# Kernel tuning notes

Hardware: AMD Instinct MI355X
Metric: run time of the kernel (lower is better)

Reference implementation:

```python
import jax, jax.numpy as jnp
import numpy as np

B, N_ATOMS = 8192, 64      # molecules, atoms per molecule
DIM, EXTRA, N_CLS = 70, 7, 11
N_FP = 10000               # fingerprint vocab


def setup_inputs() -> dict:
    key = jax.random.key(0)
    ks = jax.random.split(key, 9)
    atoms = jax.random.randint(ks[0], (B, N_ATOMS), 0, N_FP, dtype=jnp.int64 if jax.config.jax_enable_x64 else jnp.int32)
    adjacency = jax.random.uniform(ks[1], (B, N_ATOMS, N_ATOMS), dtype=jnp.float32)
    sel_desc = jax.random.normal(ks[2], (B, EXTRA), dtype=jnp.float32)
    embed_table = jax.random.normal(ks[3], (N_FP, DIM), dtype=jnp.float32)
    w1 = jax.random.normal(ks[4], (DIM, DIM), dtype=jnp.float32) * 0.05
    b1 = jax.random.normal(ks[5], (DIM,), dtype=jnp.float32) * 0.05
    w2 = jax.random.normal(ks[6], (DIM, DIM), dtype=jnp.float32) * 0.05
    b2 = jax.random.normal(ks[7], (DIM,), dtype=jnp.float32) * 0.05
    wp = jax.random.normal(ks[8], (DIM + EXTRA, N_CLS), dtype=jnp.float32) * 0.05
    bp = jnp.zeros((N_CLS,), dtype=jnp.float32)
    return {"atoms": atoms, "adjacency": adjacency, "sel_desc": sel_desc,
            "embed_table": embed_table, "w1": w1, "b1": b1,
            "w2": w2, "b2": b2, "wp": wp, "bp": bp}


def reference(atoms, adjacency, sel_desc, embed_table, w1, b1, w2, b2, wp, bp):
    # embed atoms: [B, n, dim]
    x = embed_table[atoms]
    # message-passing layers: relu(linear) then (block-diagonal == batched) adjacency matmul
    for w, b in ((w1, b1), (w2, b2)):
        h = jax.nn.relu(jnp.einsum('bnd,de->bne', x, w) + b)
        x = jnp.einsum('bnm,bmd->bnd', adjacency, h)
    # segment-sum pool over atoms per molecule (sum_axis)
    y = jnp.sum(x, axis=1)                       # [B, dim]
    y = jnp.concatenate([y, sel_desc], axis=1)   # [B, dim+extra]
    return jnp.einsum('bd,dc->bc', y, wp) + bp   # [B, 11]
```

## Files before the change

kernel.cpp:

```cpp
#include <hip/hip_runtime.h>

#define NFP   10000
#define DIM   70
#define DPAD  72
#define NATOMS 64

typedef short  short8  __attribute__((ext_vector_type(8)));
typedef float  floatx4 __attribute__((ext_vector_type(4)));

__device__ inline unsigned short f2bf(float f) {
  union { float f; unsigned u; } x; x.f = f;
  unsigned r = x.u + 0x7fffu + ((x.u >> 16) & 1u);
  return (unsigned short)(r >> 16);
}

__global__ __launch_bounds__(256) void precompute_G(
    const float* __restrict__ emb, const float* __restrict__ w1,
    const float* __restrict__ b1,  const float* __restrict__ w2,
    unsigned short* __restrict__ G) {
  __shared__ float w1s[DIM * DPAD];
  __shared__ float w2s[DIM * DPAD];
  __shared__ float b1s[DPAD];
  __shared__ float embs[32 * DPAD];
  __shared__ float e1s[32 * DPAD];
  const int t = threadIdx.x;

  for (int i = t; i < DIM * DPAD; i += 256) {
    int r = i / DPAD, c = i % DPAD;
    float v1 = 0.f, v2 = 0.f;
    if (c < DIM) { v1 = w1[r * DIM + c]; v2 = w2[r * DIM + c]; }
    w1s[i] = v1; w2s[i] = v2;
  }
  if (t < DPAD) b1s[t] = (t < DIM) ? b1[t] : 0.f;
  const int row0 = blockIdx.x * 32;
  for (int i = t; i < 32 * DPAD; i += 256) {
    int r = i / DPAD, c = i % DPAD;
    int vr = row0 + r;
    embs[i] = (vr < NFP && c < DIM) ? emb[vr * DIM + c] : 0.f;
  }
  __syncthreads();

  for (int task = t; task < 32 * 18; task += 256) {
    int r = task / 18, c4 = (task % 18) * 4;
    float4 acc = *(const float4*)&b1s[c4];
    for (int k = 0; k < DIM; k++) {
      float e = embs[r * DPAD + k];
      float4 w = *(const float4*)&w1s[k * DPAD + c4];
      acc.x = fmaf(e, w.x, acc.x); acc.y = fmaf(e, w.y, acc.y);
      acc.z = fmaf(e, w.z, acc.z); acc.w = fmaf(e, w.w, acc.w);
    }
    acc.x = fmaxf(acc.x, 0.f); acc.y = fmaxf(acc.y, 0.f);
    acc.z = fmaxf(acc.z, 0.f); acc.w = fmaxf(acc.w, 0.f);
    *(float4*)&e1s[r * DPAD + c4] = acc;
  }
  __syncthreads();

  for (int task = t; task < 32 * 18; task += 256) {
    int r = task / 18, c4 = (task % 18) * 4;
    int vr = row0 + r;
    if (vr >= NFP) continue;
    float ax = 0.f, ay = 0.f, az = 0.f, aw = 0.f;
    for (int k = 0; k < DIM; k++) {
      float e = e1s[r * DPAD + k];
      float4 w = *(const float4*)&w2s[k * DPAD + c4];
      ax = fmaf(e, w.x, ax); ay = fmaf(e, w.y, ay);
      az = fmaf(e, w.z, az); aw = fmaf(e, w.w, aw);
    }
    unsigned short* gp = G + vr * DPAD + c4;
    gp[0] = f2bf(ax); gp[1] = f2bf(ay); gp[2] = f2bf(az); gp[3] = f2bf(aw);
  }
}

__global__ __launch_bounds__(256) void mol_fused(
    const int* __restrict__ atoms, const float* __restrict__ adj,
    const float* __restrict__ sel, const float* __restrict__ b2,
    const float* __restrict__ wp,  const float* __restrict__ bp,
    const unsigned short* __restrict__ G, float* __restrict__ out) {
  __shared__ unsigned short adjs[64 * DPAD];
  __shared__ unsigned short gTs[80 * DPAD];
  __shared__ float cpart[16 * 64];
  __shared__ float cvec[64];
  __shared__ float b2p[80];
  __shared__ float yacc[16 * 80];
  __shared__ float yv[80];
  __shared__ int   satoms[64];

  const int b = blockIdx.x;
  const int t = threadIdx.x;

  if (t < 64) satoms[t] = atoms[b * 64 + t];
  if (t < 80) b2p[t] = (t < DIM) ? b2[t] : 0.f;
  __syncthreads();

  {
    const float* ap = adj + (size_t)b * 4096;
    const int mc = (t & 15) * 4;
    const int a  = t >> 4;
    float4 cs = make_float4(0.f, 0.f, 0.f, 0.f);
#pragma unroll
    for (int it = 0; it < 4; it++) {
      int n = a + 16 * it;
      float4 v = *(const float4*)(ap + n * 64 + mc);
      cs.x += v.x; cs.y += v.y; cs.z += v.z; cs.w += v.w;
      ushort4 u;
      u.x = f2bf(v.x); u.y = f2bf(v.y); u.z = f2bf(v.z); u.w = f2bf(v.w);
      *(ushort4*)&adjs[n * DPAD + mc] = u;
    }
    *(float4*)&cpart[a * 64 + mc] = cs;
  }

  {
    const int m = t & 63;
    const int row = satoms[m];
    const uint4* Gv = (const uint4*)G;
    for (int ch = (t >> 6); ch < 9; ch += 4) {
      uint4 v = Gv[row * 9 + ch];
      unsigned short* gp = &gTs[(ch * 8) * DPAD + m];
      gp[0 * DPAD] = (unsigned short)(v.x & 0xffff);
      gp[1 * DPAD] = (unsigned short)(v.x >> 16);
      gp[2 * DPAD] = (unsigned short)(v.y & 0xffff);
      gp[3 * DPAD] = (unsigned short)(v.y >> 16);
      gp[4 * DPAD] = (unsigned short)(v.z & 0xffff);
      gp[5 * DPAD] = (unsigned short)(v.z >> 16);
      gp[6 * DPAD] = (unsigned short)(v.w & 0xffff);
      gp[7 * DPAD] = (unsigned short)(v.w >> 16);
    }
    for (int i = t; i < 8 * DPAD; i += 256) gTs[72 * DPAD + i] = 0;
  }
  __syncthreads();

  if (t < 64) {
    float s = 0.f;
#pragma unroll
    for (int a = 0; a < 16; a++) s += cpart[a * 64 + t];
    cvec[t] = s;
  }

  const int w = t >> 6, lane = t & 63;
  const int q = lane >> 4, li = lane & 15;
  const int R = w * 16;
  short8 a0 = *(const short8*)&adjs[(R + li) * DPAD + q * 8];
  short8 a1 = *(const short8*)&adjs[(R + li) * DPAD + 32 + q * 8];
  floatx4 acc[5];
#pragma unroll
  for (int nt = 0; nt < 5; nt++) {
    floatx4 z = {0.f, 0.f, 0.f, 0.f};
    short8 b0 = *(const short8*)&gTs[(nt * 16 + li) * DPAD + q * 8];
    short8 b1 = *(const short8*)&gTs[(nt * 16 + li) * DPAD + 32 + q * 8];
    z = __builtin_amdgcn_mfma_f32_16x16x32_bf16(a0, b0, z, 0, 0, 0);
    z = __builtin_amdgcn_mfma_f32_16x16x32_bf16(a1, b1, z, 0, 0, 0);
    acc[nt] = z;
  }
  __syncthreads();

#pragma unroll
  for (int nt = 0; nt < 5; nt++) {
    int d = nt * 16 + li;
    float bb = b2p[d];
    float ps = 0.f;
#pragma unroll
    for (int r = 0; r < 4; r++) {
      float h = fmaxf(acc[nt][r] + bb, 0.f);
      ps = fmaf(cvec[R + q * 4 + r], h, ps);
    }
    yacc[(w * 4 + q) * 80 + d] = ps;
  }
  __syncthreads();

  if (t < 80) {
    float s = 0.f;
#pragma unroll
    for (int i = 0; i < 16; i++) s += yacc[i * 80 + t];
    yv[t] = (t < DIM) ? s : ((t < DIM + 7) ? sel[b * 7 + (t - DIM)] : 0.f);
  }
  __syncthreads();

  if (t < 11) {
    float s = bp[t];
    for (int d = 0; d < 77; d++) s = fmaf(yv[d], wp[d * 11 + t], s);
    out[b * 11 + t] = s;
  }
}

extern "C" void kernel_launch(void* const* d_in, const int* in_sizes, int n_in,
                              void* d_out, int out_size, void* d_ws, size_t ws_size,
                              hipStream_t stream) {
  const int*   atoms = (const int*)d_in[0];
  const float* adj   = (const float*)d_in[1];
  const float* sel   = (const float*)d_in[2];
  const float* emb   = (const float*)d_in[3];
  const float* w1    = (const float*)d_in[4];
  const float* b1    = (const float*)d_in[5];
  const float* w2    = (const float*)d_in[6];
  const float* b2    = (const float*)d_in[7];
  const float* wp    = (const float*)d_in[8];
  const float* bp    = (const float*)d_in[9];

  const int B = in_sizes[0] / NATOMS;
  unsigned short* G = (unsigned short*)d_ws;

  precompute_G<<<(NFP + 31) / 32, 256, 0, stream>>>(emb, w1, b1, w2, G);
  mol_fused<<<B, 256, 0, stream>>>(atoms, adj, sel, b2, wp, bp, G, (float*)d_out);
}
```

Baseline: 255.2 us.

## Split final projection into separate kernel and use shuffle reductions

Moves the final 77x11 projection out of the per-molecule kernel into a separate batched kernel that reads pooled vectors from workspace. This removes the serial 11-thread tail and two block barriers from each molecule block. Column-sum and per-feature partial reductions now use wave shuffles instead of shared-memory staging, and the bf16 conversion uses a packed intrinsic. The cost is an extra kernel launch plus a workspace round trip for the pooled vectors.

```diff
diff --git a/kernel.cpp b/kernel.cpp
--- a/kernel.cpp
+++ b/kernel.cpp
@@ -1,4 +1,5 @@
 #include <hip/hip_runtime.h>
+#include <hip/hip_bf16.h>
 
 #define NFP   10000
 #define DIM   70
@@ -12,6 +13,11 @@
   union { float f; unsigned u; } x; x.f = f;
   unsigned r = x.u + 0x7fffu + ((x.u >> 16) & 1u);
   return (unsigned short)(r >> 16);
+}
+
+__device__ inline ushort2 pk2bf(float a, float b) {
+  __hip_bfloat162 h = __float22bfloat162_rn(make_float2(a, b));
+  union { __hip_bfloat162 h; ushort2 u; } c; c.h = h; return c.u;
 }
 
 __global__ __launch_bounds__(256) void precompute_G(
@@ -73,20 +79,20 @@
 
 __global__ __launch_bounds__(256) void mol_fused(
     const int* __restrict__ atoms, const float* __restrict__ adj,
-    const float* __restrict__ sel, const float* __restrict__ b2,
-    const float* __restrict__ wp,  const float* __restrict__ bp,
-    const unsigned short* __restrict__ G, float* __restrict__ out) {
+    const float* __restrict__ b2,  const unsigned short* __restrict__ G,
+    float* __restrict__ yws) {
   __shared__ unsigned short adjs[64 * DPAD];
   __shared__ unsigned short gTs[80 * DPAD];
-  __shared__ float cpart[16 * 64];
+  __shared__ float cwave[4 * 64];
   __shared__ float cvec[64];
   __shared__ float b2p[80];
-  __shared__ float yacc[16 * 80];
-  __shared__ float yv[80];
+  __shared__ float yacc[4 * 80];
   __shared__ int   satoms[64];
 
   const int b = blockIdx.x;
   const int t = threadIdx.x;
+  const int w = t >> 6, lane = t & 63;
+  const int q = lane >> 4, li = lane & 15;
 
   if (t < 64) satoms[t] = atoms[b * 64 + t];
   if (t < 80) b2p[t] = (t < DIM) ? b2[t] : 0.f;
@@ -102,18 +108,24 @@
       int n = a + 16 * it;
       float4 v = *(const float4*)(ap + n * 64 + mc);
       cs.x += v.x; cs.y += v.y; cs.z += v.z; cs.w += v.w;
-      ushort4 u;
-      u.x = f2bf(v.x); u.y = f2bf(v.y); u.z = f2bf(v.z); u.w = f2bf(v.w);
+      ushort2 lo = pk2bf(v.x, v.y);
+      ushort2 hi = pk2bf(v.z, v.w);
+      ushort4 u; u.x = lo.x; u.y = lo.y; u.z = hi.x; u.w = hi.y;
       *(ushort4*)&adjs[n * DPAD + mc] = u;
     }
-    *(float4*)&cpart[a * 64 + mc] = cs;
+#pragma unroll
+    for (int s = 16; s <= 32; s <<= 1) {
+      cs.x += __shfl_xor(cs.x, s); cs.y += __shfl_xor(cs.y, s);
+      cs.z += __shfl_xor(cs.z, s); cs.w += __shfl_xor(cs.w, s);
+    }
+    if (((t >> 4) & 3) == 0) *(float4*)&cwave[w * 64 + mc] = cs;
   }
 
   {
     const int m = t & 63;
     const int row = satoms[m];
     const uint4* Gv = (const uint4*)G;
-    for (int ch = (t >> 6); ch < 9; ch += 4) {
+    for (int ch = w; ch < 9; ch += 4) {
       uint4 v = Gv[row * 9 + ch];
       unsigned short* gp = &gTs[(ch * 8) * DPAD + m];
       gp[0 * DPAD] = (unsigned short)(v.x & 0xffff);
@@ -130,14 +142,9 @@
   __syncthreads();
 
   if (t < 64) {
-    float s = 0.f;
-#pragma unroll
-    for (int a = 0; a < 16; a++) s += cpart[a * 64 + t];
-    cvec[t] = s;
-  }
-
-  const int w = t >> 6, lane = t & 63;
-  const int q = lane >> 4, li = lane & 15;
+    cvec[t] = cwave[t] + cwave[64 + t] + cwave[128 + t] + cwave[192 + t];
+  }
+
   const int R = w * 16;
   short8 a0 = *(const short8*)&adjs[(R + li) * DPAD + q * 8];
   short8 a1 = *(const short8*)&adjs[(R + li) * DPAD + 32 + q * 8];
@@ -153,33 +160,54 @@
   }
   __syncthreads();
 
+  float ps[5];
 #pragma unroll
   for (int nt = 0; nt < 5; nt++) {
     int d = nt * 16 + li;
     float bb = b2p[d];
-    float ps = 0.f;
+    float p = 0.f;
 #pragma unroll
     for (int r = 0; r < 4; r++) {
       float h = fmaxf(acc[nt][r] + bb, 0.f);
-      ps = fmaf(cvec[R + q * 4 + r], h, ps);
-    }
-    yacc[(w * 4 + q) * 80 + d] = ps;
-  }
-  __syncthreads();
-
-  if (t < 80) {
-    float s = 0.f;
-#pragma unroll
-    for (int i = 0; i < 16; i++) s += yacc[i * 80 + t];
-    yv[t] = (t < DIM) ? s : ((t < DIM + 7) ? sel[b * 7 + (t - DIM)] : 0.f);
-  }
-  __syncthreads();
-
-  if (t < 11) {
-    float s = bp[t];
-    for (int d = 0; d < 77; d++) s = fmaf(yv[d], wp[d * 11 + t], s);
-    out[b * 11 + t] = s;
-  }
+      p = fmaf(cvec[R + q * 4 + r], h, p);
+    }
+    p += __shfl_xor(p, 16);
+    p += __shfl_xor(p, 32);
+    ps[nt] = p;
+  }
+  if (q == 0) {
+#pragma unroll
+    for (int nt = 0; nt < 5; nt++) yacc[w * 80 + nt * 16 + li] = ps[nt];
+  }
+  __syncthreads();
+
+  if (t < DIM) {
+    float s = yacc[t] + yacc[80 + t] + yacc[160 + t] + yacc[240 + t];
+    yws[(size_t)b * DIM + t] = s;
+  }
+}
+
+__global__ __launch_bounds__(256) void proj_out(
+    const float* __restrict__ yws, const float* __restrict__ sel,
+    const float* __restrict__ wp,  const float* __restrict__ bp,
+    float* __restrict__ out, int B) {
+  __shared__ float wps[77 * 11];
+  __shared__ float bps[11];
+  const int t = threadIdx.x;
+  for (int i = t; i < 77 * 11; i += 256) wps[i] = wp[i];
+  if (t < 11) bps[t] = bp[t];
+  __syncthreads();
+  const int gid = blockIdx.x * 256 + t;
+  if (gid >= B * 11) return;
+  const int b = gid / 11, c = gid % 11;
+  float s = bps[c];
+  const float* yp = yws + (size_t)b * DIM;
+#pragma unroll 7
+  for (int d = 0; d < DIM; d++) s = fmaf(yp[d], wps[d * 11 + c], s);
+  const float* sp = sel + (size_t)b * 7;
+#pragma unroll
+  for (int d = 0; d < 7; d++) s = fmaf(sp[d], wps[(DIM + d) * 11 + c], s);
+  out[gid] = s;
 }
 
 extern "C" void kernel_launch(void* const* d_in, const int* in_sizes, int n_in,
@@ -198,7 +226,9 @@
 
   const int B = in_sizes[0] / NATOMS;
   unsigned short* G = (unsigned short*)d_ws;
+  float* yws = (float*)((char*)d_ws + (2 << 20));
 
   precompute_G<<<(NFP + 31) / 32, 256, 0, stream>>>(emb, w1, b1, w2, G);
-  mol_fused<<<B, 256, 0, stream>>>(atoms, adj, sel, b2, wp, bp, G, (float*)d_out);
-}
+  mol_fused<<<B, 256, 0, stream>>>(atoms, adj, b2, G, yws);
+  proj_out<<<(B * 11 + 255) / 256, 256, 0, stream>>>(yws, sel, wp, bp, (float*)d_out, B);
+}
```

Result: no change. 255.1 us (-0.0%).
